# Performance work log

Measured on AMD Instinct MI355X. Metric: run time of the kernel, lower is better.

## Reference

```python
import jax, jax.numpy as jnp
import numpy as np

INTER = 30
NPOOL = 33            # int(1000/30), matches AvgPool2d floor behavior
CA_SCALE = NPOOL ** 0.5
EMB, HEADS, DEPTH = 10, 5, 3


def _ln(x, g, b, eps=1e-5):
    m = jnp.mean(x, -1, keepdims=True)
    v = jnp.mean(jnp.square(x - m), -1, keepdims=True)
    return (x - m) * jax.lax.rsqrt(v + eps) * g + b


def _pool(x):
    # AvgPool2d(kernel=(1,INTER), stride=(1,INTER)) on last dim: [b,o,c,s] -> [b,o,c,NPOOL]
    b, o, c, s = x.shape
    return x[..., :NPOOL * INTER].reshape(b, o, c, NPOOL, INTER).mean(-1)


def _conv(x, w, strides):
    return jax.lax.conv_general_dilated(x, w, strides, 'VALID',
                                        dimension_numbers=('NCHW', 'OIHW', 'NCHW'))


def _channel_attention(x, qw, qb, qg, qbe, kw, kb, kg, kbe, pw, pb, pg, pbe):
    temp = jnp.swapaxes(x, -1, -2)                               # b o s c
    q = jnp.swapaxes(_ln(temp @ qw + qb, qg, qbe), -1, -2)       # b o c s
    k = jnp.swapaxes(_ln(temp @ kw + kb, kg, kbe), -1, -2)
    att = jnp.einsum('bocs,boms->bocm', _pool(q), _pool(k)) / CA_SCALE
    score = jax.nn.softmax(att, axis=-1)
    out = jnp.einsum('bocs,bocm->bocs', x, score)                # m summed out, as in torch einsum
    out = _ln(jnp.swapaxes(out, -1, -2) @ pw + pb, pg, pbe)
    return jnp.swapaxes(out, -1, -2)


def _mha(x, qw, qb, kw, kb, vw, vb, ow, ob):
    b, n, e = x.shape
    d = e // HEADS
    q = (x @ qw + qb).reshape(b, n, HEADS, d).transpose(0, 2, 1, 3)
    k = (x @ kw + kb).reshape(b, n, HEADS, d).transpose(0, 2, 1, 3)
    v = (x @ vw + vb).reshape(b, n, HEADS, d).transpose(0, 2, 1, 3)
    energy = jnp.einsum('bhqd,bhkd->bhqk', q, k)
    att = jax.nn.softmax(energy / (e ** 0.5), axis=-1)
    out = jnp.einsum('bhqk,bhkd->bhqd', att, v)
    return out.transpose(0, 2, 1, 3).reshape(b, n, e) @ ow + ob


def setup_inputs():
    key = jax.random.key(0)
    ks = jax.random.split(key, 16)
    g = lambda i, sh, s=0.1: jax.random.normal(ks[i], sh, jnp.float32) * s
    z = lambda sh: jnp.zeros(sh, jnp.float32)
    o = lambda sh: jnp.ones(sh, jnp.float32)
    return dict(
        x=jax.random.normal(ks[0], (512, 1, 1000, 22), jnp.float32),
        change_w=g(1, (22, 16)), change_b=z((16,)),
        ca_q_w=g(2, (16, 16)), ca_q_b=z((16,)), ca_q_g=o((16,)), ca_q_be=z((16,)),
        ca_k_w=g(3, (16, 16)), ca_k_b=z((16,)), ca_k_g=o((16,)), ca_k_be=z((16,)),
        ca_p_w=g(4, (16, 16)), ca_p_b=z((16,)), ca_p_g=o((16,)), ca_p_be=z((16,)),
        conv1_w=g(5, (2, 1, 1, 51)), conv1_b=z((2,)),
        bn_g=o((2,)), bn_b=z((2,)), bn_mean=z((2,)), bn_var=o((2,)),
        conv2_w=g(6, (10, 2, 16, 5)), conv2_b=z((10,)),
        tf_ln1_g=o((3, 10)), tf_ln1_b=z((3, 10)),
        tf_q_w=g(7, (3, 10, 10)), tf_q_b=z((3, 10)),
        tf_k_w=g(8, (3, 10, 10)), tf_k_b=z((3, 10)),
        tf_v_w=g(9, (3, 10, 10)), tf_v_b=z((3, 10)),
        tf_o_w=g(10, (3, 10, 10)), tf_o_b=z((3, 10)),
        tf_ln2_g=o((3, 10)), tf_ln2_b=z((3, 10)),
        tf_ff1_w=g(11, (3, 10, 40)), tf_ff1_b=z((3, 40)),
        tf_ff2_w=g(12, (3, 40, 10)), tf_ff2_b=z((3, 10)),
    )


def reference(x, change_w, change_b,
              ca_q_w, ca_q_b, ca_q_g, ca_q_be,
              ca_k_w, ca_k_b, ca_k_g, ca_k_be,
              ca_p_w, ca_p_b, ca_p_g, ca_p_be,
              conv1_w, conv1_b, bn_g, bn_b, bn_mean, bn_var,
              conv2_w, conv2_b,
              tf_ln1_g, tf_ln1_b, tf_q_w, tf_q_b, tf_k_w, tf_k_b,
              tf_v_w, tf_v_b, tf_o_w, tf_o_b, tf_ln2_g, tf_ln2_b,
              tf_ff1_w, tf_ff1_b, tf_ff2_w, tf_ff2_b):
    h = x @ change_w + change_b                  # [b,1,1000,16]
    h = jnp.swapaxes(h, -1, -2)                  # [b,1,16,1000]
    for _ in range(4):
        h = _channel_attention(h, ca_q_w, ca_q_b, ca_q_g, ca_q_be,
                               ca_k_w, ca_k_b, ca_k_g, ca_k_be,
                               ca_p_w, ca_p_b, ca_p_g, ca_p_be) + h
    c = _conv(h, conv1_w, (1, 1)) + conv1_b[None, :, None, None]     # [b,2,16,950]
    bshape = lambda v: v[None, :, None, None]
    c = (c - bshape(bn_mean)) * bshape(jax.lax.rsqrt(bn_var + 1e-5)) * bshape(bn_g) + bshape(bn_b)
    c = jnp.where(c > 0, c, 0.2 * c)             # LeakyReLU(0.2)
    c = _conv(c, conv2_w, (1, 5)) + conv2_b[None, :, None, None]     # [b,10,1,190]
    b_, e_, hh, ww = c.shape
    t = c.reshape(b_, e_, hh * ww).transpose(0, 2, 1)                # [b,190,10]
    for i in range(DEPTH):
        y = _ln(t, tf_ln1_g[i], tf_ln1_b[i])
        t = t + _mha(y, tf_q_w[i], tf_q_b[i], tf_k_w[i], tf_k_b[i],
                     tf_v_w[i], tf_v_b[i], tf_o_w[i], tf_o_b[i])
        y = _ln(t, tf_ln2_g[i], tf_ln2_b[i])
        t = t + (jax.nn.gelu(y @ tf_ff1_w[i] + tf_ff1_b[i], approximate=False) @ tf_ff2_w[i] + tf_ff2_b[i])
    return t
```

## Files before the change

### kernel.cpp

```cpp
#include <hip/hip_runtime.h>

typedef unsigned short ushort_t;

__device__ __forceinline__ float u2f(ushort_t u){
    union{unsigned int i; float f;} x; x.i = ((unsigned int)u) << 16; return x.f;
}
__device__ __forceinline__ ushort_t f2u(float f){
    union{float fl; unsigned int i;} x; x.fl = f;
    unsigned int r = x.i + 0x7FFFu + ((x.i >> 16) & 1u);
    return (ushort_t)(r >> 16);
}

#define REP10(M) M(0)M(1)M(2)M(3)M(4)M(5)M(6)M(7)M(8)M(9)
#define REP16(M) M(0)M(1)M(2)M(3)M(4)M(5)M(6)M(7)M(8)M(9)M(10)M(11)M(12)M(13)M(14)M(15)
#define REP22(M) REP16(M) M(16)M(17)M(18)M(19)M(20)M(21)
#define REP55(M) M(0)M(1)M(2)M(3)M(4)M(5)M(6)M(7)M(8)M(9)M(10)M(11)M(12)M(13)M(14)M(15)M(16)M(17)M(18)M(19)M(20)M(21)M(22)M(23)M(24)M(25)M(26)M(27)M(28)M(29)M(30)M(31)M(32)M(33)M(34)M(35)M(36)M(37)M(38)M(39)M(40)M(41)M(42)M(43)M(44)M(45)M(46)M(47)M(48)M(49)M(50)M(51)M(52)M(53)M(54)

__global__ __launch_bounds__(256)
void k_embed(const float* __restrict__ X,
             const float* __restrict__ CW, const float* __restrict__ CB,
             const float* __restrict__ PW, const float* __restrict__ PB,
             const float* __restrict__ PG, const float* __restrict__ PBE,
             ushort_t* __restrict__ Hws)
{
    const int idx = blockIdx.x * 256 + threadIdx.x;
    const int b = idx / 1000, s = idx - b * 1000;
    const float* xp = X + (size_t)idx * 22;

#define E_DX(j) float x##j = xp[j];
    REP22(E_DX)
#define E_DV(c) float v##c = CB[c];
    REP16(E_DV)
#define E_CH(j) { const float xx = x##j; const float* w = CW + (j)*16; \
    v0+=xx*w[0]; v1+=xx*w[1]; v2+=xx*w[2]; v3+=xx*w[3]; \
    v4+=xx*w[4]; v5+=xx*w[5]; v6+=xx*w[6]; v7+=xx*w[7]; \
    v8+=xx*w[8]; v9+=xx*w[9]; v10+=xx*w[10]; v11+=xx*w[11]; \
    v12+=xx*w[12]; v13+=xx*w[13]; v14+=xx*w[14]; v15+=xx*w[15]; }
    REP22(E_CH)

#define E_DU(c) float u##c = PB[c];
#define E_PJ(j) { const float vv = v##j; const float* w = PW + (j)*16; \
    u0+=vv*w[0]; u1+=vv*w[1]; u2+=vv*w[2]; u3+=vv*w[3]; \
    u4+=vv*w[4]; u5+=vv*w[5]; u6+=vv*w[6]; u7+=vv*w[7]; \
    u8+=vv*w[8]; u9+=vv*w[9]; u10+=vv*w[10]; u11+=vv*w[11]; \
    u12+=vv*w[12]; u13+=vv*w[13]; u14+=vv*w[14]; u15+=vv*w[15]; }
#define E_DS(c) const float d##c = u##c - m;
#define E_UP(c) v##c += d##c * inv * PG[c] + PBE[c];
#define E_LNIT { \
    REP16(E_DU) REP16(E_PJ) \
    float m = (((u0+u1)+(u2+u3))+((u4+u5)+(u6+u7)))+(((u8+u9)+(u10+u11))+((u12+u13)+(u14+u15))); \
    m *= 0.0625f; \
    REP16(E_DS) \
    float var = (((d0*d0+d1*d1)+(d2*d2+d3*d3))+((d4*d4+d5*d5)+(d6*d6+d7*d7)))+(((d8*d8+d9*d9)+(d10*d10+d11*d11))+((d12*d12+d13*d13)+(d14*d14+d15*d15))); \
    var *= 0.0625f; \
    float inv = rsqrtf(var + 1e-5f); \
    REP16(E_UP) }

    E_LNIT E_LNIT E_LNIT E_LNIT

    ushort_t* hp = Hws + b*16000 + s;
#define E_ST(c) hp[(c)*1000] = f2u(v##c);
    REP16(E_ST)
}

__global__ __launch_bounds__(256)
void k_conv(const ushort_t* __restrict__ Hws,
            const float* __restrict__ W1, const float* __restrict__ B1,
            const float* __restrict__ BNG, const float* __restrict__ BNB,
            const float* __restrict__ BNM, const float* __restrict__ BNV,
            const float* __restrict__ W2, const float* __restrict__ B2,
            float* __restrict__ Tws)
{
    __shared__ ushort_t sH[16000];
    const int tid = threadIdx.x, b = blockIdx.x;

    {
        const unsigned int* src = (const unsigned int*)(Hws + b*16000);
        unsigned int* dst = (unsigned int*)sH;
        for (int i = tid; i < 8000; i += 256) dst[i] = src[i];
    }
    const float sc0 = BNG[0]*rsqrtf(BNV[0]+1e-5f);
    const float sc1 = BNG[1]*rsqrtf(BNV[1]+1e-5f);
    const float sh0 = BNB[0] + (B1[0]-BNM[0])*sc0;
    const float sh1 = BNB[1] + (B1[1]-BNM[1])*sc1;
    __syncthreads();

    if (tid < 190){
        const int w5 = tid*5;
#define C_DT(o) float t##o = B2[o];
        REP10(C_DT)
        const float* w1a = W1;
        const float* w1b = W1 + 51;
        for (int kh = 0; kh < 16; ++kh){
            const ushort_t* hp = sH + kh*1000 + w5;
            float a0=0.f,a1=0.f,a2=0.f,a3=0.f,a4=0.f;
            float b0_=0.f,b1_=0.f,b2_=0.f,b3_=0.f,b4_=0.f;
#define C_TAP(e) { const float cur = u2f(hp[e]); \
            if ((e) < 51)              { a0+=cur*w1a[(e)];   b0_+=cur*w1b[(e)];   } \
            if ((e) >= 1 && (e) < 52)  { a1+=cur*w1a[(e)-1]; b1_+=cur*w1b[(e)-1]; } \
            if ((e) >= 2 && (e) < 53)  { a2+=cur*w1a[(e)-2]; b2_+=cur*w1b[(e)-2]; } \
            if ((e) >= 3 && (e) < 54)  { a3+=cur*w1a[(e)-3]; b3_+=cur*w1b[(e)-3]; } \
            if ((e) >= 4)              { a4+=cur*w1a[(e)-4]; b4_+=cur*w1b[(e)-4]; } }
            REP55(C_TAP)
#define C_LR(q) { a##q = a##q*sc0 + sh0; a##q = a##q > 0.f ? a##q : 0.2f*a##q; \
                  b##q##_ = b##q##_*sc1 + sh1; b##q##_ = b##q##_ > 0.f ? b##q##_ : 0.2f*b##q##_; }
            C_LR(0) C_LR(1) C_LR(2) C_LR(3) C_LR(4)
#define C_C2(o) { const float* wa = W2 + (((o)*2  )*16 + kh)*5; \
                  const float* wb = W2 + (((o)*2+1)*16 + kh)*5; \
        t##o += a0*wa[0]+a1*wa[1]+a2*wa[2]+a3*wa[3]+a4*wa[4] \
              + b0_*wb[0]+b1_*wb[1]+b2_*wb[2]+b3_*wb[3]+b4_*wb[4]; }
            REP10(C_C2)
        }
        float* op = Tws + (size_t)b*1900 + tid*10;
#define C_ST(o) op[o] = t##o;
        REP10(C_ST)
    }
}

__global__ __launch_bounds__(256)
void k_tf(const float* __restrict__ Tws,
          const float* __restrict__ LN1G, const float* __restrict__ LN1B,
          const float* __restrict__ QW, const float* __restrict__ QBv,
          const float* __restrict__ KW, const float* __restrict__ KBv,
          const float* __restrict__ VW, const float* __restrict__ VBv,
          const float* __restrict__ OW, const float* __restrict__ OBv,
          const float* __restrict__ LN2G, const float* __restrict__ LN2B,
          const float* __restrict__ F1W, const float* __restrict__ F1B,
          const float* __restrict__ F2W, const float* __restrict__ F2B,
          float* __restrict__ OUT)
{
    __shared__ __align__(16) float T [190*11];
    __shared__ __align__(16) float QB[190*12];
    __shared__ __align__(16) float KB[190*12];
    __shared__ __align__(16) float VB[190*12];
    __shared__ __align__(16) float AT[190*12];

    const int tid = threadIdx.x, b = blockIdx.x;
    for (int i = tid; i < 1900; i += 256){
        int r = i/10, c = i - r*10;
        T[r*11 + c] = Tws[(size_t)b*1900 + i];
    }
    __syncthreads();

    const float SCALE = 0.31622776601683794f;
    const bool act = (tid < 190);
#pragma unroll 1
    for (int L = 0; L < 3; ++L){
        const float* ln1g = LN1G + L*10; const float* ln1b = LN1B + L*10;
        const float* qw = QW + L*100;    const float* qb = QBv + L*10;
        const float* kw = KW + L*100;    const float* kb = KBv + L*10;
        const float* vw = VW + L*100;    const float* vb = VBv + L*10;
        const float* ow = OW + L*100;    const float* ob = OBv + L*10;
        const float* ln2g = LN2G + L*10; const float* ln2b = LN2B + L*10;
        const float* f1w = F1W + L*400;  const float* f1b = F1B + L*40;
        const float* f2w = F2W + L*400;  const float* f2b = F2B + L*10;

        if (act){
#define T_TV(c) float tv##c = T[tid*11 + c];
            REP10(T_TV)
            float m = (((tv0+tv1)+(tv2+tv3))+((tv4+tv5)+(tv6+tv7)))+(tv8+tv9);
            m *= 0.1f;
#define T_D1(c) const float e1##c = tv##c - m;
            REP10(T_D1)
            float var = (((e10*e10+e11*e11)+(e12*e12+e13*e13))+((e14*e14+e15*e15)+(e16*e16+e17*e17)))+(e18*e18+e19*e19);
            var *= 0.1f;
            float inv = rsqrtf(var + 1e-5f);
#define T_Y(c) const float y##c = e1##c*inv*ln1g[c] + ln1b[c];
            REP10(T_Y)
#define T_PQ(c) { float aq = qb[c] + y0*qw[c] + y1*qw[10+c] + y2*qw[20+c] + y3*qw[30+c] + y4*qw[40+c] \
                           + y5*qw[50+c] + y6*qw[60+c] + y7*qw[70+c] + y8*qw[80+c] + y9*qw[90+c]; \
                  QB[tid*12 + c] = aq; }
            REP10(T_PQ)
#define T_PK(c) { float ak = kb[c] + y0*kw[c] + y1*kw[10+c] + y2*kw[20+c] + y3*kw[30+c] + y4*kw[40+c] \
                           + y5*kw[50+c] + y6*kw[60+c] + y7*kw[70+c] + y8*kw[80+c] + y9*kw[90+c]; \
                  KB[tid*12 + c] = ak; }
            REP10(T_PK)
#define T_PV(c) { float av = vb[c] + y0*vw[c] + y1*vw[10+c] + y2*vw[20+c] + y3*vw[30+c] + y4*vw[40+c] \
                           + y5*vw[50+c] + y6*vw[60+c] + y7*vw[70+c] + y8*vw[80+c] + y9*vw[90+c]; \
                  VB[tid*12 + c] = av; }
            REP10(T_PV)
        }
        __syncthreads();

        if (tid < 240){
            const int h5 = tid / 48;
            const int qg = tid - h5*48;
            const int q0 = qg * 4;
#define T_LQ(i) float qx##i, qy##i; { const int qi = q0 + i; \
            if (qi < 190){ qx##i = QB[qi*12 + 2*h5]*SCALE; qy##i = QB[qi*12 + 2*h5 + 1]*SCALE; } \
            else { qx##i = 0.f; qy##i = 0.f; } }
            T_LQ(0) T_LQ(1) T_LQ(2) T_LQ(3)
            float l0=0.f,l1=0.f,l2=0.f,l3=0.f;
            float p00=0.f,p01=0.f,p10=0.f,p11=0.f,p20=0.f,p21=0.f,p30=0.f,p31=0.f;
            const float* kp = KB + 2*h5;
            const float* vp = VB + 2*h5;
            for (int kk = 0; kk < 190; ++kk){
                const float2 kv = *(const float2*)(kp + kk*12);
                const float2 vv = *(const float2*)(vp + kk*12);
                const float e0 = __expf(qx0*kv.x + qy0*kv.y);
                const float e1 = __expf(qx1*kv.x + qy1*kv.y);
                const float e2 = __expf(qx2*kv.x + qy2*kv.y);
                const float e3 = __expf(qx3*kv.x + qy3*kv.y);
                l0 += e0; p00 += e0*vv.x; p01 += e0*vv.y;
                l1 += e1; p10 += e1*vv.x; p11 += e1*vv.y;
                l2 += e2; p20 += e2*vv.x; p21 += e2*vv.y;
                l3 += e3; p30 += e3*vv.x; p31 += e3*vv.y;
            }
#define T_SA(i) { const int qi = q0 + i; if (qi < 190){ const float rl = 1.f/l##i; \
                  AT[qi*12 + 2*h5] = p##i##0*rl; AT[qi*12 + 2*h5 + 1] = p##i##1*rl; } }
            T_SA(0) T_SA(1) T_SA(2) T_SA(3)
        }
        __syncthreads();

        if (act){
#define T_TV2(c) float w##c = T[tid*11 + c];
            REP10(T_TV2)
#define T_AT(c) const float at##c = AT[tid*12 + c];
            REP10(T_AT)
#define T_OP(c) w##c += ob[c] + at0*ow[c] + at1*ow[10+c] + at2*ow[20+c] + at3*ow[30+c] + at4*ow[40+c] \
                       + at5*ow[50+c] + at6*ow[60+c] + at7*ow[70+c] + at8*ow[80+c] + at9*ow[90+c];
            REP10(T_OP)
            float m2 = (((w0+w1)+(w2+w3))+((w4+w5)+(w6+w7)))+(w8+w9);
            m2 *= 0.1f;
#define T_D2(c) const float e2##c = w##c - m2;
            REP10(T_D2)
            float var2 = (((e20*e20+e21*e21)+(e22*e22+e23*e23))+((e24*e24+e25*e25)+(e26*e26+e27*e27)))+(e28*e28+e29*e29);
            var2 *= 0.1f;
            float inv2 = rsqrtf(var2 + 1e-5f);
#define T_Z(c) const float z##c = e2##c*inv2*ln2g[c] + ln2b[c];
            REP10(T_Z)
#define T_DD(c) float dd##c = f2b[c];
            REP10(T_DD)
#pragma unroll 4
            for (int j = 0; j < 40; ++j){
                float aj = f1b[j] + z0*f1w[j] + z1*f1w[40+j] + z2*f1w[80+j] + z3*f1w[120+j] + z4*f1w[160+j]
                         + z5*f1w[200+j] + z6*f1w[240+j] + z7*f1w[280+j] + z8*f1w[320+j] + z9*f1w[360+j];
                const float gj = 0.5f * aj * (1.f + erff(aj * 0.70710678118654752f));
                const float* w2p = f2w + j*10;
                dd0 += gj*w2p[0]; dd1 += gj*w2p[1]; dd2 += gj*w2p[2]; dd3 += gj*w2p[3]; dd4 += gj*w2p[4];
                dd5 += gj*w2p[5]; dd6 += gj*w2p[6]; dd7 += gj*w2p[7]; dd8 += gj*w2p[8]; dd9 += gj*w2p[9];
            }
#define T_WB(c) T[tid*11 + c] = w##c + dd##c;
            REP10(T_WB)
        }
        __syncthreads();
    }

    if (act){
        float* op = OUT + (size_t)b*1900 + tid*10;
#define T_OUT(c) op[c] = T[tid*11 + c];
        REP10(T_OUT)
    }
}

extern "C" void kernel_launch(void* const* d_in, const int* in_sizes, int n_in,
                              void* d_out, int out_size, void* d_ws, size_t ws_size,
                              hipStream_t stream)
{
    (void)ws_size; (void)n_in; (void)out_size;
    const int B = in_sizes[0] / 22000;
    auto in = [&](int i){ return (const float*)d_in[i]; };
    ushort_t* Hws = (ushort_t*)d_ws;
    float*    Tws = (float*)((char*)d_ws + (size_t)B*16000*2);

    k_embed<<<(B*1000 + 255)/256, 256, 0, stream>>>(
        in(0), in(1), in(2), in(11), in(12), in(13), in(14), Hws);

    k_conv<<<B, 256, 0, stream>>>(
        Hws, in(15), in(16), in(17), in(18), in(19), in(20), in(21), in(22), Tws);

    k_tf<<<B, 256, 0, stream>>>(
        Tws,
        in(23), in(24), in(25), in(26), in(27), in(28), in(29), in(30),
        in(31), in(32), in(33), in(34), in(35), in(36), in(37), in(38),
        (float*)d_out);
}
```

Before: 398.9 us.

## Stage embed input via LDS, widen conv copy, pack attention math into float2 vectors

```diff
diff --git a/kernel.cpp b/kernel.cpp
--- a/kernel.cpp
+++ b/kernel.cpp
@@ -1,6 +1,7 @@
 #include <hip/hip_runtime.h>
 
 typedef unsigned short ushort_t;
+typedef float v2f __attribute__((ext_vector_type(2)));
 
 __device__ __forceinline__ float u2f(ushort_t u){
     union{unsigned int i; float f;} x; x.i = ((unsigned int)u) << 16; return x.f;
@@ -23,11 +24,25 @@
              const float* __restrict__ PG, const float* __restrict__ PBE,
              ushort_t* __restrict__ Hws)
 {
-    const int idx = blockIdx.x * 256 + threadIdx.x;
+    __shared__ float sX[256*23];
+    const int t = threadIdx.x;
+    const int base = blockIdx.x * 256;
+
+    {
+        const float2* src = (const float2*)(X + (size_t)base * 22);
+        for (int i = t; i < 2816; i += 256){
+            int r = i / 11, c = (i - r*11) * 2;
+            float2 v = src[i];
+            sX[r*23 + c] = v.x; sX[r*23 + c + 1] = v.y;
+        }
+    }
+    __syncthreads();
+
+    const int idx = base + t;
     const int b = idx / 1000, s = idx - b * 1000;
-    const float* xp = X + (size_t)idx * 22;
-
-#define E_DX(j) float x##j = xp[j];
+    const float* xp = sX + t*23;
+
+#define E_DX(j) const float x##j = xp[j];
     REP22(E_DX)
 #define E_DV(c) float v##c = CB[c];
     REP16(E_DV)
@@ -75,9 +90,9 @@
     const int tid = threadIdx.x, b = blockIdx.x;
 
     {
-        const unsigned int* src = (const unsigned int*)(Hws + b*16000);
-        unsigned int* dst = (unsigned int*)sH;
-        for (int i = tid; i < 8000; i += 256) dst[i] = src[i];
+        const uint4* src = (const uint4*)(Hws + b*16000);
+        uint4* dst = (uint4*)sH;
+        for (int i = tid; i < 2000; i += 256) dst[i] = src[i];
     }
     const float sc0 = BNG[0]*rsqrtf(BNV[0]+1e-5f);
     const float sc1 = BNG[1]*rsqrtf(BNV[1]+1e-5f);
@@ -142,7 +157,7 @@
     }
     __syncthreads();
 
-    const float SCALE = 0.31622776601683794f;
+    const float LSCALE = (float)(0.31622776601683794 * 1.4426950408889634);
     const bool act = (tid < 190);
 #pragma unroll 1
     for (int L = 0; L < 3; ++L){
@@ -187,28 +202,33 @@
             const int qg = tid - h5*48;
             const int q0 = qg * 4;
 #define T_LQ(i) float qx##i, qy##i; { const int qi = q0 + i; \
-            if (qi < 190){ qx##i = QB[qi*12 + 2*h5]*SCALE; qy##i = QB[qi*12 + 2*h5 + 1]*SCALE; } \
+            if (qi < 190){ qx##i = QB[qi*12 + 2*h5]*LSCALE; qy##i = QB[qi*12 + 2*h5 + 1]*LSCALE; } \
             else { qx##i = 0.f; qy##i = 0.f; } }
             T_LQ(0) T_LQ(1) T_LQ(2) T_LQ(3)
-            float l0=0.f,l1=0.f,l2=0.f,l3=0.f;
-            float p00=0.f,p01=0.f,p10=0.f,p11=0.f,p20=0.f,p21=0.f,p30=0.f,p31=0.f;
+            v2f qxA = {qx0, qx1}, qxB = {qx2, qx3};
+            v2f qyA = {qy0, qy1}, qyB = {qy2, qy3};
+            v2f lA = {0.f,0.f}, lB = {0.f,0.f};
+            v2f pxA = {0.f,0.f}, pxB = {0.f,0.f};
+            v2f pyA = {0.f,0.f}, pyB = {0.f,0.f};
             const float* kp = KB + 2*h5;
             const float* vp = VB + 2*h5;
             for (int kk = 0; kk < 190; ++kk){
                 const float2 kv = *(const float2*)(kp + kk*12);
                 const float2 vv = *(const float2*)(vp + kk*12);
-                const float e0 = __expf(qx0*kv.x + qy0*kv.y);
-                const float e1 = __expf(qx1*kv.x + qy1*kv.y);
-                const float e2 = __expf(qx2*kv.x + qy2*kv.y);
-                const float e3 = __expf(qx3*kv.x + qy3*kv.y);
-                l0 += e0; p00 += e0*vv.x; p01 += e0*vv.y;
-                l1 += e1; p10 += e1*vv.x; p11 += e1*vv.y;
-                l2 += e2; p20 += e2*vv.x; p21 += e2*vv.y;
-                l3 += e3; p30 += e3*vv.x; p31 += e3*vv.y;
+                const v2f kx = {kv.x, kv.x}, ky = {kv.y, kv.y};
+                v2f dA = qxA*kx + qyA*ky;
+                v2f dB = qxB*kx + qyB*ky;
+                v2f eA = {exp2f(dA.x), exp2f(dA.y)};
+                v2f eB = {exp2f(dB.x), exp2f(dB.y)};
+                lA += eA; lB += eB;
+                const v2f vx = {vv.x, vv.x}, vy = {vv.y, vv.y};
+                pxA += eA*vx; pxB += eB*vx;
+                pyA += eA*vy; pyB += eB*vy;
             }
-#define T_SA(i) { const int qi = q0 + i; if (qi < 190){ const float rl = 1.f/l##i; \
-                  AT[qi*12 + 2*h5] = p##i##0*rl; AT[qi*12 + 2*h5 + 1] = p##i##1*rl; } }
-            T_SA(0) T_SA(1) T_SA(2) T_SA(3)
+#define T_SA(i, vec, fld) { const int qi = q0 + i; if (qi < 190){ \
+                const float rl = 1.f/l##vec.fld; \
+                AT[qi*12 + 2*h5] = px##vec.fld*rl; AT[qi*12 + 2*h5 + 1] = py##vec.fld*rl; } }
+            T_SA(0, A, x) T_SA(1, A, y) T_SA(2, B, x) T_SA(3, B, y)
         }
         __syncthreads();
 
```

New measurement: 413.8 us. 1.04x slower.

## Stage weights and inputs in shared memory, vectorize loads, use exp2 in attention

Applied to the files above, without the earlier changes.

```diff
diff --git a/kernel.cpp b/kernel.cpp
--- a/kernel.cpp
+++ b/kernel.cpp
@@ -23,44 +23,87 @@
              const float* __restrict__ PG, const float* __restrict__ PBE,
              ushort_t* __restrict__ Hws)
 {
-    const int idx = blockIdx.x * 256 + threadIdx.x;
-    const int b = idx / 1000, s = idx - b * 1000;
-    const float* xp = X + (size_t)idx * 22;
-
-#define E_DX(j) float x##j = xp[j];
-    REP22(E_DX)
-#define E_DV(c) float v##c = CB[c];
+    __shared__ __align__(16) float sW[672];
+    __shared__ __align__(16) float sX[512*23];
+    const int t = threadIdx.x;
+    const int base = blockIdx.x * 512;
+
+    for (int i = t; i < 352; i += 256) sW[i] = CW[i];
+    for (int i = t; i < 256; i += 256) sW[368+i] = PW[i];
+    if (t < 16){ sW[352+t]=CB[t]; sW[624+t]=PB[t]; sW[640+t]=PG[t]; sW[656+t]=PBE[t]; }
+    {
+        const float2* src = (const float2*)(X + (size_t)base*22);
+        for (int i = t; i < 5632; i += 256){
+            int r = i/11, c = (i - r*11)*2;
+            float2 v = src[i];
+            sX[r*23+c] = v.x; sX[r*23+c+1] = v.y;
+        }
+    }
+    __syncthreads();
+
+    const float* xa = sX + t*23;
+    const float* xb = sX + (t+256)*23;
+
+#define E_DV(c) float va##c, vb##c; { const float b0 = sW[352+(c)]; va##c=b0; vb##c=b0; }
     REP16(E_DV)
-#define E_CH(j) { const float xx = x##j; const float* w = CW + (j)*16; \
-    v0+=xx*w[0]; v1+=xx*w[1]; v2+=xx*w[2]; v3+=xx*w[3]; \
-    v4+=xx*w[4]; v5+=xx*w[5]; v6+=xx*w[6]; v7+=xx*w[7]; \
-    v8+=xx*w[8]; v9+=xx*w[9]; v10+=xx*w[10]; v11+=xx*w[11]; \
-    v12+=xx*w[12]; v13+=xx*w[13]; v14+=xx*w[14]; v15+=xx*w[15]; }
+#define E_CH(j) { const float4 wA = *(const float4*)(sW+(j)*16); \
+    const float4 wB = *(const float4*)(sW+(j)*16+4); \
+    const float4 wC = *(const float4*)(sW+(j)*16+8); \
+    const float4 wD = *(const float4*)(sW+(j)*16+12); \
+    const float xA = xa[j], xB = xb[j]; \
+    va0+=xA*wA.x; va1+=xA*wA.y; va2+=xA*wA.z; va3+=xA*wA.w; \
+    va4+=xA*wB.x; va5+=xA*wB.y; va6+=xA*wB.z; va7+=xA*wB.w; \
+    va8+=xA*wC.x; va9+=xA*wC.y; va10+=xA*wC.z; va11+=xA*wC.w; \
+    va12+=xA*wD.x; va13+=xA*wD.y; va14+=xA*wD.z; va15+=xA*wD.w; \
+    vb0+=xB*wA.x; vb1+=xB*wA.y; vb2+=xB*wA.z; vb3+=xB*wA.w; \
+    vb4+=xB*wB.x; vb5+=xB*wB.y; vb6+=xB*wB.z; vb7+=xB*wB.w; \
+    vb8+=xB*wC.x; vb9+=xB*wC.y; vb10+=xB*wC.z; vb11+=xB*wC.w; \
+    vb12+=xB*wD.x; vb13+=xB*wD.y; vb14+=xB*wD.z; vb15+=xB*wD.w; }
     REP22(E_CH)
 
-#define E_DU(c) float u##c = PB[c];
-#define E_PJ(j) { const float vv = v##j; const float* w = PW + (j)*16; \
-    u0+=vv*w[0]; u1+=vv*w[1]; u2+=vv*w[2]; u3+=vv*w[3]; \
-    u4+=vv*w[4]; u5+=vv*w[5]; u6+=vv*w[6]; u7+=vv*w[7]; \
-    u8+=vv*w[8]; u9+=vv*w[9]; u10+=vv*w[10]; u11+=vv*w[11]; \
-    u12+=vv*w[12]; u13+=vv*w[13]; u14+=vv*w[14]; u15+=vv*w[15]; }
-#define E_DS(c) const float d##c = u##c - m;
-#define E_UP(c) v##c += d##c * inv * PG[c] + PBE[c];
+#define E_DU(c) float ua##c, ub##c; { const float b0 = sW[624+(c)]; ua##c=b0; ub##c=b0; }
+#define E_PJ(j) { const float4 wA = *(const float4*)(sW+368+(j)*16); \
+    const float4 wB = *(const float4*)(sW+368+(j)*16+4); \
+    const float4 wC = *(const float4*)(sW+368+(j)*16+8); \
+    const float4 wD = *(const float4*)(sW+368+(j)*16+12); \
+    ua0+=va##j*wA.x; ua1+=va##j*wA.y; ua2+=va##j*wA.z; ua3+=va##j*wA.w; \
+    ua4+=va##j*wB.x; ua5+=va##j*wB.y; ua6+=va##j*wB.z; ua7+=va##j*wB.w; \
+    ua8+=va##j*wC.x; ua9+=va##j*wC.y; ua10+=va##j*wC.z; ua11+=va##j*wC.w; \
+    ua12+=va##j*wD.x; ua13+=va##j*wD.y; ua14+=va##j*wD.z; ua15+=va##j*wD.w; \
+    ub0+=vb##j*wA.x; ub1+=vb##j*wA.y; ub2+=vb##j*wA.z; ub3+=vb##j*wA.w; \
+    ub4+=vb##j*wB.x; ub5+=vb##j*wB.y; ub6+=vb##j*wB.z; ub7+=vb##j*wB.w; \
+    ub8+=vb##j*wC.x; ub9+=vb##j*wC.y; ub10+=vb##j*wC.z; ub11+=vb##j*wC.w; \
+    ub12+=vb##j*wD.x; ub13+=vb##j*wD.y; ub14+=vb##j*wD.z; ub15+=vb##j*wD.w; }
+#define E_DS(c) const float da##c = ua##c - ma; const float db##c = ub##c - mb;
+#define E_UP(c) { const float g = sW[640+(c)], be = sW[656+(c)]; \
+    va##c += da##c * inva * g + be; vb##c += db##c * invb * g + be; }
 #define E_LNIT { \
     REP16(E_DU) REP16(E_PJ) \
-    float m = (((u0+u1)+(u2+u3))+((u4+u5)+(u6+u7)))+(((u8+u9)+(u10+u11))+((u12+u13)+(u14+u15))); \
-    m *= 0.0625f; \
+    const float ma = ((((ua0+ua1)+(ua2+ua3))+((ua4+ua5)+(ua6+ua7)))+(((ua8+ua9)+(ua10+ua11))+((ua12+ua13)+(ua14+ua15))))*0.0625f; \
+    const float mb = ((((ub0+ub1)+(ub2+ub3))+((ub4+ub5)+(ub6+ub7)))+(((ub8+ub9)+(ub10+ub11))+((ub12+ub13)+(ub14+ub15))))*0.0625f; \
     REP16(E_DS) \
-    float var = (((d0*d0+d1*d1)+(d2*d2+d3*d3))+((d4*d4+d5*d5)+(d6*d6+d7*d7)))+(((d8*d8+d9*d9)+(d10*d10+d11*d11))+((d12*d12+d13*d13)+(d14*d14+d15*d15))); \
-    var *= 0.0625f; \
-    float inv = rsqrtf(var + 1e-5f); \
+    const float vara = ((((da0*da0+da1*da1)+(da2*da2+da3*da3))+((da4*da4+da5*da5)+(da6*da6+da7*da7)))+(((da8*da8+da9*da9)+(da10*da10+da11*da11))+((da12*da12+da13*da13)+(da14*da14+da15*da15))))*0.0625f; \
+    const float varb = ((((db0*db0+db1*db1)+(db2*db2+db3*db3))+((db4*db4+db5*db5)+(db6*db6+db7*db7)))+(((db8*db8+db9*db9)+(db10*db10+db11*db11))+((db12*db12+db13*db13)+(db14*db14+db15*db15))))*0.0625f; \
+    const float inva = rsqrtf(vara + 1e-5f); \
+    const float invb = rsqrtf(varb + 1e-5f); \
     REP16(E_UP) }
 
     E_LNIT E_LNIT E_LNIT E_LNIT
 
-    ushort_t* hp = Hws + b*16000 + s;
-#define E_ST(c) hp[(c)*1000] = f2u(v##c);
-    REP16(E_ST)
+    {
+        const int row0 = base + t;
+        const int b0 = row0 / 1000, s0 = row0 - b0*1000;
+        ushort_t* hp = Hws + b0*16000 + s0;
+#define E_STA(c) hp[(c)*1000] = f2u(va##c);
+        REP16(E_STA)
+    }
+    {
+        const int row1 = base + t + 256;
+        const int b1 = row1 / 1000, s1 = row1 - b1*1000;
+        ushort_t* hp = Hws + b1*16000 + s1;
+#define E_STB(c) hp[(c)*1000] = f2u(vb##c);
+        REP16(E_STB)
+    }
 }
 
 __global__ __launch_bounds__(256)
@@ -75,9 +118,9 @@
     const int tid = threadIdx.x, b = blockIdx.x;
 
     {
-        const unsigned int* src = (const unsigned int*)(Hws + b*16000);
-        unsigned int* dst = (unsigned int*)sH;
-        for (int i = tid; i < 8000; i += 256) dst[i] = src[i];
+        const uint4* src = (const uint4*)(Hws + b*16000);
+        uint4* dst = (uint4*)sH;
+        for (int i = tid; i < 2000; i += 256) dst[i] = src[i];
     }
     const float sc0 = BNG[0]*rsqrtf(BNV[0]+1e-5f);
     const float sc1 = BNG[1]*rsqrtf(BNV[1]+1e-5f);
@@ -129,6 +172,7 @@
           const float* __restrict__ F2W, const float* __restrict__ F2B,
           float* __restrict__ OUT)
 {
+    __shared__ __align__(16) float TW[3*1536];
     __shared__ __align__(16) float T [190*11];
     __shared__ __align__(16) float QB[190*12];
     __shared__ __align__(16) float KB[190*12];
@@ -136,49 +180,69 @@
     __shared__ __align__(16) float AT[190*12];
 
     const int tid = threadIdx.x, b = blockIdx.x;
+
+    for (int i = tid; i < 30; i += 256){ int L=i/10, j=i-L*10;
+        TW[L*1536 +    j] = LN1G[i];  TW[L*1536 + 12 + j] = LN1B[i];
+        TW[L*1536 +144 + j] = QBv[i]; TW[L*1536 +276 + j] = KBv[i];
+        TW[L*1536 +408 + j] = VBv[i]; TW[L*1536 +540 + j] = OBv[i];
+        TW[L*1536 +552 + j] = LN2G[i];TW[L*1536 +564 + j] = LN2B[i];
+        TW[L*1536+1496 + j] = F2B[i];
+    }
+    for (int i = tid; i < 300; i += 256){ int L=i/100, r=(i-L*100)/10, c=i%10;
+        TW[L*1536 + 24 + r*12 + c] = QW[i];
+        TW[L*1536 +156 + r*12 + c] = KW[i];
+        TW[L*1536 +288 + r*12 + c] = VW[i];
+        TW[L*1536 +420 + r*12 + c] = OW[i];
+    }
+    for (int i = tid; i < 1200; i += 256){ int L=i/400, r=i-L*400;
+        TW[L*1536 + 576 + r] = F1W[i];
+        int rr = r/10, cc = r - rr*10;
+        TW[L*1536 +1016 + rr*12 + cc] = F2W[i];
+    }
+    for (int i = tid; i < 120; i += 256){ int L=i/40, j=i-L*40;
+        TW[L*1536 + 976 + j] = F1B[i];
+    }
     for (int i = tid; i < 1900; i += 256){
         int r = i/10, c = i - r*10;
         T[r*11 + c] = Tws[(size_t)b*1900 + i];
     }
     __syncthreads();
 
-    const float SCALE = 0.31622776601683794f;
+    const float LSCALE = (float)(0.31622776601683794 * 1.4426950408889634);
     const bool act = (tid < 190);
 #pragma unroll 1
     for (int L = 0; L < 3; ++L){
-        const float* ln1g = LN1G + L*10; const float* ln1b = LN1B + L*10;
-        const float* qw = QW + L*100;    const float* qb = QBv + L*10;
-        const float* kw = KW + L*100;    const float* kb = KBv + L*10;
-        const float* vw = VW + L*100;    const float* vb = VBv + L*10;
-        const float* ow = OW + L*100;    const float* ob = OBv + L*10;
-        const float* ln2g = LN2G + L*10; const float* ln2b = LN2B + L*10;
-        const float* f1w = F1W + L*400;  const float* f1b = F1B + L*40;
-        const float* f2w = F2W + L*400;  const float* f2b = F2B + L*10;
+        const float* Wb = TW + L*1536;
 
         if (act){
 #define T_TV(c) float tv##c = T[tid*11 + c];
             REP10(T_TV)
-            float m = (((tv0+tv1)+(tv2+tv3))+((tv4+tv5)+(tv6+tv7)))+(tv8+tv9);
-            m *= 0.1f;
+            float m = ((((tv0+tv1)+(tv2+tv3))+((tv4+tv5)+(tv6+tv7)))+(tv8+tv9))*0.1f;
 #define T_D1(c) const float e1##c = tv##c - m;
             REP10(T_D1)
-            float var = (((e10*e10+e11*e11)+(e12*e12+e13*e13))+((e14*e14+e15*e15)+(e16*e16+e17*e17)))+(e18*e18+e19*e19);
-            var *= 0.1f;
+            float var = ((((e10*e10+e11*e11)+(e12*e12+e13*e13))+((e14*e14+e15*e15)+(e16*e16+e17*e17)))+(e18*e18+e19*e19))*0.1f;
             float inv = rsqrtf(var + 1e-5f);
-#define T_Y(c) const float y##c = e1##c*inv*ln1g[c] + ln1b[c];
+#define T_Y(c) const float y##c = e1##c*inv*Wb[c] + Wb[12+c];
             REP10(T_Y)
-#define T_PQ(c) { float aq = qb[c] + y0*qw[c] + y1*qw[10+c] + y2*qw[20+c] + y3*qw[30+c] + y4*qw[40+c] \
-                           + y5*qw[50+c] + y6*qw[60+c] + y7*qw[70+c] + y8*qw[80+c] + y9*qw[90+c]; \
-                  QB[tid*12 + c] = aq; }
-            REP10(T_PQ)
-#define T_PK(c) { float ak = kb[c] + y0*kw[c] + y1*kw[10+c] + y2*kw[20+c] + y3*kw[30+c] + y4*kw[40+c] \
-                           + y5*kw[50+c] + y6*kw[60+c] + y7*kw[70+c] + y8*kw[80+c] + y9*kw[90+c]; \
-                  KB[tid*12 + c] = ak; }
-            REP10(T_PK)
-#define T_PV(c) { float av = vb[c] + y0*vw[c] + y1*vw[10+c] + y2*vw[20+c] + y3*vw[30+c] + y4*vw[40+c] \
-                           + y5*vw[50+c] + y6*vw[60+c] + y7*vw[70+c] + y8*vw[80+c] + y9*vw[90+c]; \
-                  VB[tid*12 + c] = av; }
-            REP10(T_PV)
+#define T_PJ(j, WO) { const float4 wA = *(const float4*)(Wb+(WO)+(j)*12); \
+    const float4 wB_ = *(const float4*)(Wb+(WO)+(j)*12+4); \
+    const float2 wC_ = *(const float2*)(Wb+(WO)+(j)*12+8); \
+    a0+=y##j*wA.x; a1+=y##j*wA.y; a2+=y##j*wA.z; a3+=y##j*wA.w; \
+    a4+=y##j*wB_.x; a5+=y##j*wB_.y; a6+=y##j*wB_.z; a7+=y##j*wB_.w; \
+    a8+=y##j*wC_.x; a9+=y##j*wC_.y; }
+#define T_PROJ(DST, WO, BO) { \
+    float a0=Wb[(BO)+0],a1=Wb[(BO)+1],a2=Wb[(BO)+2],a3=Wb[(BO)+3],a4=Wb[(BO)+4]; \
+    float a5=Wb[(BO)+5],a6=Wb[(BO)+6],a7=Wb[(BO)+7],a8=Wb[(BO)+8],a9=Wb[(BO)+9]; \
+    T_PJ(0,WO) T_PJ(1,WO) T_PJ(2,WO) T_PJ(3,WO) T_PJ(4,WO) \
+    T_PJ(5,WO) T_PJ(6,WO) T_PJ(7,WO) T_PJ(8,WO) T_PJ(9,WO) \
+    float4 s1; s1.x=a0; s1.y=a1; s1.z=a2; s1.w=a3; \
+    float4 s2; s2.x=a4; s2.y=a5; s2.z=a6; s2.w=a7; \
+    float2 s3; s3.x=a8; s3.y=a9; \
+    *(float4*)((DST)+tid*12) = s1; *(float4*)((DST)+tid*12+4) = s2; \
+    *(float2*)((DST)+tid*12+8) = s3; }
+            T_PROJ(QB, 24, 144)
+            T_PROJ(KB, 156, 276)
+            T_PROJ(VB, 288, 408)
         }
         __syncthreads();
 
@@ -187,20 +251,21 @@
             const int qg = tid - h5*48;
             const int q0 = qg * 4;
 #define T_LQ(i) float qx##i, qy##i; { const int qi = q0 + i; \
-            if (qi < 190){ qx##i = QB[qi*12 + 2*h5]*SCALE; qy##i = QB[qi*12 + 2*h5 + 1]*SCALE; } \
+            if (qi < 190){ qx##i = QB[qi*12 + 2*h5]*LSCALE; qy##i = QB[qi*12 + 2*h5 + 1]*LSCALE; } \
             else { qx##i = 0.f; qy##i = 0.f; } }
             T_LQ(0) T_LQ(1) T_LQ(2) T_LQ(3)
             float l0=0.f,l1=0.f,l2=0.f,l3=0.f;
             float p00=0.f,p01=0.f,p10=0.f,p11=0.f,p20=0.f,p21=0.f,p30=0.f,p31=0.f;
             const float* kp = KB + 2*h5;
             const float* vp = VB + 2*h5;
+#pragma unroll 2
             for (int kk = 0; kk < 190; ++kk){
                 const float2 kv = *(const float2*)(kp + kk*12);
                 const float2 vv = *(const float2*)(vp + kk*12);
-                const float e0 = __expf(qx0*kv.x + qy0*kv.y);
-                const float e1 = __expf(qx1*kv.x + qy1*kv.y);
-                const float e2 = __expf(qx2*kv.x + qy2*kv.y);
-                const float e3 = __expf(qx3*kv.x + qy3*kv.y);
+                const float e0 = exp2f(qx0*kv.x + qy0*kv.y);
+                const float e1 = exp2f(qx1*kv.x + qy1*kv.y);
+                const float e2 = exp2f(qx2*kv.x + qy2*kv.y);
+                const float e3 = exp2f(qx3*kv.x + qy3*kv.y);
                 l0 += e0; p00 += e0*vv.x; p01 += e0*vv.y;
                 l1 += e1; p10 += e1*vv.x; p11 += e1*vv.y;
                 l2 += e2; p20 += e2*vv.x; p21 += e2*vv.y;
@@ -215,30 +280,53 @@
         if (act){
 #define T_TV2(c) float w##c = T[tid*11 + c];
             REP10(T_TV2)
-#define T_AT(c) const float at##c = AT[tid*12 + c];
-            REP10(T_AT)
-#define T_OP(c) w##c += ob[c] + at0*ow[c] + at1*ow[10+c] + at2*ow[20+c] + at3*ow[30+c] + at4*ow[40+c] \
-                       + at5*ow[50+c] + at6*ow[60+c] + at7*ow[70+c] + at8*ow[80+c] + at9*ow[90+c];
-            REP10(T_OP)
-            float m2 = (((w0+w1)+(w2+w3))+((w4+w5)+(w6+w7)))+(w8+w9);
-            m2 *= 0.1f;
+            const float4 atA = *(const float4*)(AT + tid*12);
+            const float4 atB = *(const float4*)(AT + tid*12 + 4);
+            const float2 atC = *(const float2*)(AT + tid*12 + 8);
+            const float at0=atA.x, at1=atA.y, at2=atA.z, at3=atA.w;
+            const float at4=atB.x, at5=atB.y, at6=atB.z, at7=atB.w;
+            const float at8=atC.x, at9=atC.y;
+            {
+                float a0=Wb[540+0],a1=Wb[540+1],a2=Wb[540+2],a3=Wb[540+3],a4=Wb[540+4];
+                float a5=Wb[540+5],a6=Wb[540+6],a7=Wb[540+7],a8=Wb[540+8],a9=Wb[540+9];
+#define T_PO(j) { const float4 wA = *(const float4*)(Wb+420+(j)*12); \
+    const float4 wB_ = *(const float4*)(Wb+420+(j)*12+4); \
+    const float2 wC_ = *(const float2*)(Wb+420+(j)*12+8); \
+    a0+=at##j*wA.x; a1+=at##j*wA.y; a2+=at##j*wA.z; a3+=at##j*wA.w; \
+    a4+=at##j*wB_.x; a5+=at##j*wB_.y; a6+=at##j*wB_.z; a7+=at##j*wB_.w; \
+    a8+=at##j*wC_.x; a9+=at##j*wC_.y; }
+                T_PO(0) T_PO(1) T_PO(2) T_PO(3) T_PO(4)
+                T_PO(5) T_PO(6) T_PO(7) T_PO(8) T_PO(9)
+                w0+=a0; w1+=a1; w2+=a2; w3+=a3; w4+=a4;
+                w5+=a5; w6+=a6; w7+=a7; w8+=a8; w9+=a9;
+            }
+            float m2 = ((((w0+w1)+(w2+w3))+((w4+w5)+(w6+w7)))+(w8+w9))*0.1f;
 #define T_D2(c) const float e2##c = w##c - m2;
             REP10(T_D2)
-            float var2 = (((e20*e20+e21*e21)+(e22*e22+e23*e23))+((e24*e24+e25*e25)+(e26*e26+e27*e27)))+(e28*e28+e29*e29);
-            var2 *= 0.1f;
+            float var2 = ((((e20*e20+e21*e21)+(e22*e22+e23*e23))+((e24*e24+e25*e25)+(e26*e26+e27*e27)))+(e28*e28+e29*e29))*0.1f;
             float inv2 = rsqrtf(var2 + 1e-5f);
-#define T_Z(c) const float z##c = e2##c*inv2*ln2g[c] + ln2b[c];
+#define T_Z(c) const float z##c = e2##c*inv2*Wb[552+c] + Wb[564+c];
             REP10(T_Z)
-#define T_DD(c) float dd##c = f2b[c];
+#define T_DD(c) float dd##c = Wb[1496+c];
             REP10(T_DD)
-#pragma unroll 4
-            for (int j = 0; j < 40; ++j){
-                float aj = f1b[j] + z0*f1w[j] + z1*f1w[40+j] + z2*f1w[80+j] + z3*f1w[120+j] + z4*f1w[160+j]
-                         + z5*f1w[200+j] + z6*f1w[240+j] + z7*f1w[280+j] + z8*f1w[320+j] + z9*f1w[360+j];
-                const float gj = 0.5f * aj * (1.f + erff(aj * 0.70710678118654752f));
-                const float* w2p = f2w + j*10;
-                dd0 += gj*w2p[0]; dd1 += gj*w2p[1]; dd2 += gj*w2p[2]; dd3 += gj*w2p[3]; dd4 += gj*w2p[4];
-                dd5 += gj*w2p[5]; dd6 += gj*w2p[6]; dd7 += gj*w2p[7]; dd8 += gj*w2p[8]; dd9 += gj*w2p[9];
+#pragma unroll 1
+            for (int jb = 0; jb < 10; ++jb){
+                const float* f1p = Wb + 576 + jb*4;
+                const float4 b4 = *(const float4*)(Wb + 976 + jb*4);
+                float A0=b4.x, A1=b4.y, A2=b4.z, A3=b4.w;
+#define T_FF1(c) { const float4 wc = *(const float4*)(f1p + (c)*40); \
+                A0+=z##c*wc.x; A1+=z##c*wc.y; A2+=z##c*wc.z; A3+=z##c*wc.w; }
+                REP10(T_FF1)
+#define T_G(q) const float g##q = 0.5f*A##q*(1.f + erff(A##q*0.70710678118654752f));
+                T_G(0) T_G(1) T_G(2) T_G(3)
+                const float* f2p = Wb + 1016 + jb*48;
+#define T_FF2(q) { const float4 wA = *(const float4*)(f2p + (q)*12); \
+    const float4 wB_ = *(const float4*)(f2p + (q)*12 + 4); \
+    const float2 wC_ = *(const float2*)(f2p + (q)*12 + 8); \
+    dd0+=g##q*wA.x; dd1+=g##q*wA.y; dd2+=g##q*wA.z; dd3+=g##q*wA.w; \
+    dd4+=g##q*wB_.x; dd5+=g##q*wB_.y; dd6+=g##q*wB_.z; dd7+=g##q*wB_.w; \
+    dd8+=g##q*wC_.x; dd9+=g##q*wC_.y; }
+                T_FF2(0) T_FF2(1) T_FF2(2) T_FF2(3)
             }
 #define T_WB(c) T[tid*11 + c] = w##c + dd##c;
             REP10(T_WB)
@@ -263,7 +351,7 @@
     ushort_t* Hws = (ushort_t*)d_ws;
     float*    Tws = (float*)((char*)d_ws + (size_t)B*16000*2);
 
-    k_embed<<<(B*1000 + 255)/256, 256, 0, stream>>>(
+    k_embed<<<(B*1000)/512, 256, 0, stream>>>(
         in(0), in(1), in(2), in(11), in(12), in(13), in(14), Hws);
 
     k_conv<<<B, 256, 0, stream>>>(
```

Result: slower. 452.9 us (+13.5%).
